# Optimization experiments

Measured on AMD Instinct MI355X. Metric: run time of the kernel, lower is better.

The kernel has to match this reference:

```python
import jax, jax.numpy as jnp
import numpy as np

N = 131072      # total nodes across batched molecular graphs
E = 524288      # directed edges (avg degree ~4)
G = 4096        # number of graphs in the batch
C_IN = 78       # atom feature dim
C_OUT = 128


def _init_linear(key, fan_in, fan_out):
    kw, kb = jax.random.split(key)
    s = 1.0 / np.sqrt(fan_in)
    W = jax.random.uniform(kw, (fan_in, fan_out), jnp.float32, -s, s)
    b = jax.random.uniform(kb, (fan_out,), jnp.float32, -s, s)
    return W, b


def setup_inputs() -> dict:
    key = jax.random.key(0)
    ks = jax.random.split(key, 8)
    x = jax.random.normal(ks[0], (N, C_IN), jnp.float32)
    edge_index = jax.random.randint(ks[1], (2, E), 0, N, dtype=jnp.int32)
    # sorted graph assignment, every graph non-empty (32 nodes per graph)
    batch = ((jnp.arange(N, dtype=jnp.int32) * G) // N).astype(jnp.int32)
    W1, b1 = _init_linear(ks[2], C_IN, C_IN)
    W2, b2 = _init_linear(ks[3], C_IN, 2 * C_IN)
    W3, b3 = _init_linear(ks[4], 2 * C_IN, 4 * C_IN)
    fcW, fcb = _init_linear(ks[5], 4 * C_IN, C_OUT)
    return {"x": x, "edge_index": edge_index, "batch": batch,
            "W1": W1, "b1": b1, "W2": W2, "b2": b2,
            "W3": W3, "b3": b3, "fcW": fcW, "fcb": fcb}


def _gcn_norm(edge_index, n):
    # PyG gcn_norm: add self-loops (weight 1), symmetric D^-1/2 A D^-1/2
    loop = jnp.arange(n, dtype=edge_index.dtype)
    src = jnp.concatenate([edge_index[0], loop])
    dst = jnp.concatenate([edge_index[1], loop])
    deg = jax.ops.segment_sum(jnp.ones_like(dst, jnp.float32), dst, num_segments=n)
    dis = jnp.where(deg > 0, jax.lax.rsqrt(jnp.maximum(deg, 1.0)), 0.0)
    norm = dis[src] * dis[dst]  # [E + N]
    return src, dst, norm


def _gcn_conv(h, W, b, src, dst, norm, n):
    h = h @ W                       # linear transform first (PyG order)
    msg = h[src] * norm[:, None]    # gather + edge-normalize
    agg = jax.ops.segment_sum(msg, dst, num_segments=n)  # scatter-add
    return agg + b


def reference(x, edge_index, batch, W1, b1, W2, b2, W3, b3, fcW, fcb):
    n = x.shape[0]
    src, dst, norm = _gcn_norm(edge_index, n)
    h = jax.nn.relu(_gcn_conv(x, W1, b1, src, dst, norm, n))
    h = jax.nn.relu(_gcn_conv(h, W2, b2, src, dst, norm, n))
    h = jax.nn.relu(_gcn_conv(h, W3, b3, src, dst, norm, n))
    pooled = jax.ops.segment_max(h, batch, num_segments=G)  # global max pool
    out = pooled @ fcW + fcb
    # dropout is identity in eval mode
    return out
```

## Files before the change

### kernel.cpp

```cpp
#include <hip/hip_runtime.h>

#define NN 131072
#define NE 524288
#define NG 4096

typedef __attribute__((ext_vector_type(8))) short bfx8;
typedef __attribute__((ext_vector_type(4))) float f32x4;

static __device__ __forceinline__ ushort f2bf(float f) {
    union { float f; unsigned u; } v; v.f = f;
    unsigned r = (v.u + 0x7fff + ((v.u >> 16) & 1)) >> 16;
    return (ushort)r;
}
static __device__ __forceinline__ float bf2f(short s) {
    union { unsigned u; float f; } v;
    v.u = ((unsigned)(ushort)s) << 16;
    return v.f;
}


__global__ void k_count(const int* __restrict__ dst, int* __restrict__ counts) {
    int e = blockIdx.x * blockDim.x + threadIdx.x;
    if (e < NE) atomicAdd(&counts[dst[e]], 1);
}

__global__ void k_dis(const int* __restrict__ counts, float* __restrict__ dis) {
    int i = blockIdx.x * blockDim.x + threadIdx.x;
    if (i < NN) dis[i] = rsqrtf((float)(counts[i] + 1));
}

__global__ void k_scanA(const int* __restrict__ in, int* __restrict__ out, int* __restrict__ bsum) {
    __shared__ int s[256];
    int t = threadIdx.x;
    int i = blockIdx.x * 256 + t;
    int v = in[i];
    s[t] = v;
    __syncthreads();
    for (int off = 1; off < 256; off <<= 1) {
        int x = (t >= off) ? s[t - off] : 0;
        __syncthreads();
        s[t] += x;
        __syncthreads();
    }
    out[i] = s[t] - v;
    if (t == 255) bsum[blockIdx.x] = s[t];
}

__global__ void k_scanB(int* __restrict__ bsum) {
    __shared__ int s[512];
    int t = threadIdx.x;
    int v = bsum[t];
    s[t] = v;
    __syncthreads();
    for (int off = 1; off < 512; off <<= 1) {
        int x = (t >= off) ? s[t - off] : 0;
        __syncthreads();
        s[t] += x;
        __syncthreads();
    }
    bsum[t] = s[t] - v;
}

__global__ void k_scanC(int* __restrict__ rowstart, const int* __restrict__ bsum) {
    int t = threadIdx.x;
    int i = blockIdx.x * 256 + t;
    rowstart[i] += bsum[blockIdx.x];
    if (i == 0) rowstart[NN] = NE;
}

__global__ void k_fill(const int* __restrict__ src, const int* __restrict__ dst,
                       const int* __restrict__ rowstart, int* __restrict__ cursor,
                       const float* __restrict__ dis,
                       int* __restrict__ col, float* __restrict__ wgt) {
    int e = blockIdx.x * blockDim.x + threadIdx.x;
    if (e >= NE) return;
    int s = src[e], d = dst[e];
    int pos = rowstart[d] + atomicAdd(&cursor[d], 1);
    col[pos] = s;
    wgt[pos] = dis[s] * dis[d];
}

template<int CI, int CO, int KP>
__global__ void k_prepW(const float* __restrict__ W, ushort* __restrict__ WT) {
    int idx = blockIdx.x * 256 + threadIdx.x;
    if (idx >= CO * KP) return;
    int n = idx / KP, k = idx - n * KP;
    float v = (k < CI) ? W[k * CO + n] : 0.0f;
    WT[idx] = f2bf(v);
}

__global__ void k_prepX(const float* __restrict__ x, ushort* __restrict__ xb) {
    int idx = blockIdx.x * 256 + threadIdx.x;
    int i = idx / 96, c = idx - i * 96;
    xb[idx] = (c < 78) ? f2bf(x[i * 78 + c]) : (ushort)0;
}


template<int CP>
__global__ __launch_bounds__(256)
void k_agg8(const ushort* __restrict__ hin, const int* __restrict__ rowstart,
            const int* __restrict__ col, const float* __restrict__ wgt,
            const float* __restrict__ dis, ushort* __restrict__ out) {
    constexpr int CH = CP / 8;
    int idx = blockIdx.x * 256 + threadIdx.x;
    int i = idx / CH;
    int ch = (idx - i * CH) * 8;
    const ushort* base = hin + ch;

    float d = dis[i];
    bfx8 self = *(const bfx8*)(hin + (size_t)i * CP + ch);
    float acc[8];
    #pragma unroll
    for (int k = 0; k < 8; ++k) acc[k] = d * d * bf2f(self[k]);

    int j = rowstart[i], j1 = rowstart[i + 1];
    for (; j + 4 <= j1; j += 4) {
        int c0 = col[j], c1 = col[j + 1], c2 = col[j + 2], c3 = col[j + 3];
        float w0 = wgt[j], w1 = wgt[j + 1], w2 = wgt[j + 2], w3 = wgt[j + 3];
        bfx8 g0 = *(const bfx8*)(base + (size_t)c0 * CP);
        bfx8 g1 = *(const bfx8*)(base + (size_t)c1 * CP);
        bfx8 g2 = *(const bfx8*)(base + (size_t)c2 * CP);
        bfx8 g3 = *(const bfx8*)(base + (size_t)c3 * CP);
        #pragma unroll
        for (int k = 0; k < 8; ++k) {
            acc[k] = fmaf(w0, bf2f(g0[k]), acc[k]);
            acc[k] = fmaf(w1, bf2f(g1[k]), acc[k]);
            acc[k] = fmaf(w2, bf2f(g2[k]), acc[k]);
            acc[k] = fmaf(w3, bf2f(g3[k]), acc[k]);
        }
    }
    for (; j < j1; ++j) {
        int c = col[j];
        float w = wgt[j];
        bfx8 g = *(const bfx8*)(base + (size_t)c * CP);
        #pragma unroll
        for (int k = 0; k < 8; ++k) acc[k] = fmaf(w, bf2f(g[k]), acc[k]);
    }

    bfx8 ov;
    #pragma unroll
    for (int k = 0; k < 8; ++k) ov[k] = (short)f2bf(acc[k]);
    *(bfx8*)(out + (size_t)i * CP + ch) = ov;
}


template<int KP, int LCH, int CO, int CPO, bool POOL>
__global__ __launch_bounds__(256)
void k_mfma(const ushort* __restrict__ A, const ushort* __restrict__ BT,
            const float* __restrict__ bias, const int* __restrict__ batch,
            ushort* __restrict__ hout, float* __restrict__ pooled) {
    constexpr int NCH = KP / 8;
    constexpr int LP  = LCH * 8;
    constexpr int NP  = (CO + 63) / 64;
    __shared__ ushort sA[64 * LP];

    const int tid  = threadIdx.x;
    const int row0 = blockIdx.x * 64;

    for (int id = tid; id < 64 * NCH; id += 256) {
        int r = id / NCH, kc = id - r * NCH;
        int swz = (kc & ~7) | ((kc & 7) ^ (r & 7));
        ((int4*)(sA + r * LP))[swz] = ((const int4*)(A + (size_t)(row0 + r) * KP))[kc];
    }
    __syncthreads();

    const int lane = tid & 63;
    const int wave = tid >> 6;
    const int wr = wave >> 1, wc = wave & 1;
    const int l15 = lane & 15, l4 = lane >> 4;
    const int r7 = l15 & 7;
    const int rowA0 = wr * 32 + l15;
    const int gbase = row0 + wr * 32;
    const int koff = l4 * 8;

    #pragma unroll
    for (int p = 0; p < NP; ++p) {
        const int bc0 = p * 64 + wc * 32 + l15;
        f32x4 acc[2][2] = {};
        #pragma unroll
        for (int ks = 0; ks < KP / 32; ++ks) {
            int chunk = l4 + ks * 4;
            int swz = (chunk & ~7) | ((chunk & 7) ^ r7);
            int off = swz * 8;
            bfx8 a0 = *(const bfx8*)(sA + rowA0 * LP + off);
            bfx8 a1 = *(const bfx8*)(sA + (rowA0 + 16) * LP + off);
            bfx8 b0 = {0,0,0,0,0,0,0,0}, b1 = {0,0,0,0,0,0,0,0};
            if (bc0 < CO)      b0 = *(const bfx8*)(BT + (size_t)bc0 * KP + koff + ks * 32);
            if (bc0 + 16 < CO) b1 = *(const bfx8*)(BT + (size_t)(bc0 + 16) * KP + koff + ks * 32);
            acc[0][0] = __builtin_amdgcn_mfma_f32_16x16x32_bf16(a0, b0, acc[0][0], 0, 0, 0);
            acc[0][1] = __builtin_amdgcn_mfma_f32_16x16x32_bf16(a0, b1, acc[0][1], 0, 0, 0);
            acc[1][0] = __builtin_amdgcn_mfma_f32_16x16x32_bf16(a1, b0, acc[1][0], 0, 0, 0);
            acc[1][1] = __builtin_amdgcn_mfma_f32_16x16x32_bf16(a1, b1, acc[1][1], 0, 0, 0);
        }

        if constexpr (POOL) {
            const bool uni = (batch[gbase] == batch[gbase + 31]);
            #pragma unroll
            for (int fn = 0; fn < 2; ++fn) {
                int cg = p * 64 + wc * 32 + fn * 16 + l15;
                bool cok = cg < CO;
                float bs = cok ? bias[cg] : 0.0f;
                if (uni) {
                    float m = -1e30f;
                    #pragma unroll
                    for (int fm = 0; fm < 2; ++fm)
                        #pragma unroll
                        for (int j = 0; j < 4; ++j)
                            m = fmaxf(m, acc[fm][fn][j]);
                    m = fmaxf(m, __shfl_xor(m, 16));
                    m = fmaxf(m, __shfl_xor(m, 32));
                    if (l4 == 0 && cok) {
                        int g = batch[gbase];
                        float v = fmaxf(m + bs, 0.0f);
                        atomicMax((int*)&pooled[g * CO + cg], __float_as_int(v));
                    }
                } else {
                    #pragma unroll
                    for (int fm = 0; fm < 2; ++fm)
                        #pragma unroll
                        for (int j = 0; j < 4; ++j) {
                            if (cok) {
                                int rg = gbase + fm * 16 + l4 * 4 + j;
                                int g = batch[rg];
                                float v = fmaxf(acc[fm][fn][j] + bs, 0.0f);
                                atomicMax((int*)&pooled[g * CO + cg], __float_as_int(v));
                            }
                        }
                }
            }
        } else {
            #pragma unroll
            for (int fn = 0; fn < 2; ++fn) {
                int cg = p * 64 + wc * 32 + fn * 16 + l15;
                if (cg >= CPO) continue;
                float bs = (cg < CO) ? bias[cg] : 0.0f;
                #pragma unroll
                for (int fm = 0; fm < 2; ++fm)
                    #pragma unroll
                    for (int j = 0; j < 4; ++j) {
                        int row = gbase + fm * 16 + l4 * 4 + j;
                        float v = (cg < CO) ? fmaxf(acc[fm][fn][j] + bs, 0.0f) : 0.0f;
                        hout[(size_t)row * CPO + cg] = f2bf(v);
                    }
            }
        }
    }
}


__global__ __launch_bounds__(256)
void k_fc(const float* __restrict__ pooled, const float* __restrict__ fcW,
          const float* __restrict__ fcb, float* __restrict__ out) {
    __shared__ float sp[8][312];
    const int tid = threadIdx.x;
    const int g0 = blockIdx.x * 8;

    for (int k = tid; k < 8 * 312; k += 256)
        ((float*)sp)[k] = pooled[(size_t)g0 * 312 + k];
    __syncthreads();

    const int half = tid >> 7;
    const int c = tid & 127;
    float b = fcb[c];
    float acc0 = b, acc1 = b, acc2 = b, acc3 = b;
    const float* wp = fcW + c;
    const float* p0 = sp[half * 4 + 0];
    const float* p1 = sp[half * 4 + 1];
    const float* p2 = sp[half * 4 + 2];
    const float* p3 = sp[half * 4 + 3];
    #pragma unroll 4
    for (int k = 0; k < 312; ++k) {
        float w = wp[(size_t)k * 128];
        acc0 = fmaf(p0[k], w, acc0);
        acc1 = fmaf(p1[k], w, acc1);
        acc2 = fmaf(p2[k], w, acc2);
        acc3 = fmaf(p3[k], w, acc3);
    }
    float* o = out + (size_t)(g0 + half * 4) * 128 + c;
    o[0] = acc0; o[128] = acc1; o[256] = acc2; o[384] = acc3;
}


extern "C" void kernel_launch(void* const* d_in, const int* in_sizes, int n_in,
                              void* d_out, int out_size, void* d_ws, size_t ws_size,
                              hipStream_t stream) {
    const float* x    = (const float*)d_in[0];
    const int*   ei   = (const int*)d_in[1];
    const int*   srcv = ei;
    const int*   dstv = ei + NE;
    const int*   batch = (const int*)d_in[2];
    const float* W1 = (const float*)d_in[3];
    const float* b1 = (const float*)d_in[4];
    const float* W2 = (const float*)d_in[5];
    const float* b2 = (const float*)d_in[6];
    const float* W3 = (const float*)d_in[7];
    const float* b3 = (const float*)d_in[8];
    const float* fcW = (const float*)d_in[9];
    const float* fcb = (const float*)d_in[10];
    float* out = (float*)d_out;

    char* ws = (char*)d_ws;
    size_t off = 0;
    auto take = [&](size_t bytes) -> void* {
        void* p = ws + off;
        off += (bytes + 255) & ~(size_t)255;
        return p;
    };
    int*    counts   = (int*)take((size_t)NN * 4);
    int*    rowstart = (int*)take((size_t)(NN + 1) * 4);
    int*    cursor   = (int*)take((size_t)NN * 4);
    float*  dis      = (float*)take((size_t)NN * 4);
    int*    bsum     = (int*)take(512 * 4);
    int*    col      = (int*)take((size_t)NE * 4);
    float*  wgt      = (float*)take((size_t)NE * 4);
    ushort* R1       = (ushort*)take((size_t)NN * 160 * 2);
    ushort* R2       = (ushort*)take((size_t)NN * 160 * 2);
    ushort* R3       = (ushort*)take((size_t)NN * 96 * 2);
    float*  pooled   = (float*)take((size_t)NG * 312 * 4);
    ushort* W1T      = (ushort*)take((size_t)78 * 96 * 2);
    ushort* W2T      = (ushort*)take((size_t)156 * 96 * 2);
    ushort* W3T      = (ushort*)take((size_t)312 * 160 * 2);

    ushort* xb = R1;
    ushort* A1 = R2;
    ushort* h1 = R3;
    ushort* A2 = R1;
    ushort* h2 = R2;
    ushort* A3 = R1;

    hipMemsetAsync(counts, 0, (size_t)NN * 4, stream);
    hipMemsetAsync(cursor, 0, (size_t)NN * 4, stream);
    hipMemsetAsync(pooled, 0, (size_t)NG * 312 * 4, stream);

    k_count<<<NE / 256, 256, 0, stream>>>(dstv, counts);
    k_dis<<<NN / 256, 256, 0, stream>>>(counts, dis);
    k_scanA<<<NN / 256, 256, 0, stream>>>(counts, rowstart, bsum);
    k_scanB<<<1, 512, 0, stream>>>(bsum);
    k_scanC<<<NN / 256, 256, 0, stream>>>(rowstart, bsum);
    k_fill<<<NE / 256, 256, 0, stream>>>(srcv, dstv, rowstart, cursor, dis, col, wgt);

    k_prepW<78, 78, 96><<<(78 * 96 + 255) / 256, 256, 0, stream>>>(W1, W1T);
    k_prepW<78, 156, 96><<<(156 * 96 + 255) / 256, 256, 0, stream>>>(W2, W2T);
    k_prepW<156, 312, 160><<<(312 * 160 + 255) / 256, 256, 0, stream>>>(W3, W3T);
    k_prepX<<<NN * 96 / 256, 256, 0, stream>>>(x, xb);

    k_agg8<96><<<NN * 12 / 256, 256, 0, stream>>>(xb, rowstart, col, wgt, dis, A1);
    k_mfma<96, 16, 78, 96, false><<<NN / 64, 256, 0, stream>>>(A1, W1T, b1, nullptr, h1, nullptr);
    k_agg8<96><<<NN * 12 / 256, 256, 0, stream>>>(h1, rowstart, col, wgt, dis, A2);
    k_mfma<96, 16, 156, 160, false><<<NN / 64, 256, 0, stream>>>(A2, W2T, b2, nullptr, h2, nullptr);
    k_agg8<160><<<NN * 20 / 256, 256, 0, stream>>>(h2, rowstart, col, wgt, dis, A3);
    k_mfma<160, 24, 312, 312, true><<<NN / 64, 256, 0, stream>>>(A3, W3T, b3, batch, nullptr, pooled);
    k_fc<<<NG / 8, 256, 0, stream>>>(pooled, fcW, fcb, out);
}
```

Baseline: 381.0 us.

## Fuse neighbor aggregation into MFMA GEMM kernel via shared-memory staging

The sparse aggregation step is now computed directly inside each GEMM block. Each thread gathers neighbor rows, accumulates them, and writes the aggregated bf16 tile into the swizzled shared-memory A tile, with no separate aggregate buffer in global memory. This removes one kernel launch per layer and a full write and re-read of the aggregated activations. In exchange, the gather phase now runs with the GEMM block's occupancy and thread mapping (64 rows per block), which may give less latency hiding for the irregular gathers.

```diff
diff --git a/kernel.cpp b/kernel.cpp
--- a/kernel.cpp
+++ b/kernel.cpp
@@ -96,59 +96,14 @@
 }
 
 
-template<int CP>
-__global__ __launch_bounds__(256)
-void k_agg8(const ushort* __restrict__ hin, const int* __restrict__ rowstart,
-            const int* __restrict__ col, const float* __restrict__ wgt,
-            const float* __restrict__ dis, ushort* __restrict__ out) {
-    constexpr int CH = CP / 8;
-    int idx = blockIdx.x * 256 + threadIdx.x;
-    int i = idx / CH;
-    int ch = (idx - i * CH) * 8;
-    const ushort* base = hin + ch;
-
-    float d = dis[i];
-    bfx8 self = *(const bfx8*)(hin + (size_t)i * CP + ch);
-    float acc[8];
-    #pragma unroll
-    for (int k = 0; k < 8; ++k) acc[k] = d * d * bf2f(self[k]);
-
-    int j = rowstart[i], j1 = rowstart[i + 1];
-    for (; j + 4 <= j1; j += 4) {
-        int c0 = col[j], c1 = col[j + 1], c2 = col[j + 2], c3 = col[j + 3];
-        float w0 = wgt[j], w1 = wgt[j + 1], w2 = wgt[j + 2], w3 = wgt[j + 3];
-        bfx8 g0 = *(const bfx8*)(base + (size_t)c0 * CP);
-        bfx8 g1 = *(const bfx8*)(base + (size_t)c1 * CP);
-        bfx8 g2 = *(const bfx8*)(base + (size_t)c2 * CP);
-        bfx8 g3 = *(const bfx8*)(base + (size_t)c3 * CP);
-        #pragma unroll
-        for (int k = 0; k < 8; ++k) {
-            acc[k] = fmaf(w0, bf2f(g0[k]), acc[k]);
-            acc[k] = fmaf(w1, bf2f(g1[k]), acc[k]);
-            acc[k] = fmaf(w2, bf2f(g2[k]), acc[k]);
-            acc[k] = fmaf(w3, bf2f(g3[k]), acc[k]);
-        }
-    }
-    for (; j < j1; ++j) {
-        int c = col[j];
-        float w = wgt[j];
-        bfx8 g = *(const bfx8*)(base + (size_t)c * CP);
-        #pragma unroll
-        for (int k = 0; k < 8; ++k) acc[k] = fmaf(w, bf2f(g[k]), acc[k]);
-    }
-
-    bfx8 ov;
-    #pragma unroll
-    for (int k = 0; k < 8; ++k) ov[k] = (short)f2bf(acc[k]);
-    *(bfx8*)(out + (size_t)i * CP + ch) = ov;
-}
-
-
 template<int KP, int LCH, int CO, int CPO, bool POOL>
 __global__ __launch_bounds__(256)
-void k_mfma(const ushort* __restrict__ A, const ushort* __restrict__ BT,
-            const float* __restrict__ bias, const int* __restrict__ batch,
-            ushort* __restrict__ hout, float* __restrict__ pooled) {
+void k_fused(const ushort* __restrict__ hin, const int* __restrict__ rowstart,
+             const int* __restrict__ col, const float* __restrict__ wgt,
+             const float* __restrict__ dis,
+             const ushort* __restrict__ BT, const float* __restrict__ bias,
+             const int* __restrict__ batch,
+             ushort* __restrict__ hout, float* __restrict__ pooled) {
     constexpr int NCH = KP / 8;
     constexpr int LP  = LCH * 8;
     constexpr int NP  = (CO + 63) / 64;
@@ -158,9 +113,46 @@
     const int row0 = blockIdx.x * 64;
 
     for (int id = tid; id < 64 * NCH; id += 256) {
-        int r = id / NCH, kc = id - r * NCH;
+        int r  = id / NCH, kc = id - r * NCH;
+        int i  = row0 + r;
+        int ch = kc * 8;
+        const ushort* gb = hin + ch;
+
+        float d = dis[i];
+        bfx8 self = *(const bfx8*)(hin + (size_t)i * KP + ch);
+        float acc[8];
+        #pragma unroll
+        for (int k = 0; k < 8; ++k) acc[k] = d * d * bf2f(self[k]);
+
+        int j = rowstart[i], j1 = rowstart[i + 1];
+        for (; j + 4 <= j1; j += 4) {
+            int c0 = col[j], c1 = col[j + 1], c2 = col[j + 2], c3 = col[j + 3];
+            float w0 = wgt[j], w1 = wgt[j + 1], w2 = wgt[j + 2], w3 = wgt[j + 3];
+            bfx8 g0 = *(const bfx8*)(gb + (size_t)c0 * KP);
+            bfx8 g1 = *(const bfx8*)(gb + (size_t)c1 * KP);
+            bfx8 g2 = *(const bfx8*)(gb + (size_t)c2 * KP);
+            bfx8 g3 = *(const bfx8*)(gb + (size_t)c3 * KP);
+            #pragma unroll
+            for (int k = 0; k < 8; ++k) {
+                acc[k] = fmaf(w0, bf2f(g0[k]), acc[k]);
+                acc[k] = fmaf(w1, bf2f(g1[k]), acc[k]);
+                acc[k] = fmaf(w2, bf2f(g2[k]), acc[k]);
+                acc[k] = fmaf(w3, bf2f(g3[k]), acc[k]);
+            }
+        }
+        for (; j < j1; ++j) {
+            int c = col[j];
+            float w = wgt[j];
+            bfx8 g = *(const bfx8*)(gb + (size_t)c * KP);
+            #pragma unroll
+            for (int k = 0; k < 8; ++k) acc[k] = fmaf(w, bf2f(g[k]), acc[k]);
+        }
+
+        bfx8 ov;
+        #pragma unroll
+        for (int k = 0; k < 8; ++k) ov[k] = (short)f2bf(acc[k]);
         int swz = (kc & ~7) | ((kc & 7) ^ (r & 7));
-        ((int4*)(sA + r * LP))[swz] = ((const int4*)(A + (size_t)(row0 + r) * KP))[kc];
+        *(bfx8*)(sA + r * LP + swz * 8) = ov;
     }
     __syncthreads();
 
@@ -313,20 +305,13 @@
     int*    bsum     = (int*)take(512 * 4);
     int*    col      = (int*)take((size_t)NE * 4);
     float*  wgt      = (float*)take((size_t)NE * 4);
-    ushort* R1       = (ushort*)take((size_t)NN * 160 * 2);
-    ushort* R2       = (ushort*)take((size_t)NN * 160 * 2);
-    ushort* R3       = (ushort*)take((size_t)NN * 96 * 2);
+    ushort* xb       = (ushort*)take((size_t)NN * 96 * 2);
+    ushort* h1       = (ushort*)take((size_t)NN * 96 * 2);
+    ushort* h2       = (ushort*)take((size_t)NN * 160 * 2);
     float*  pooled   = (float*)take((size_t)NG * 312 * 4);
     ushort* W1T      = (ushort*)take((size_t)78 * 96 * 2);
     ushort* W2T      = (ushort*)take((size_t)156 * 96 * 2);
     ushort* W3T      = (ushort*)take((size_t)312 * 160 * 2);
-
-    ushort* xb = R1;
-    ushort* A1 = R2;
-    ushort* h1 = R3;
-    ushort* A2 = R1;
-    ushort* h2 = R2;
-    ushort* A3 = R1;
 
     hipMemsetAsync(counts, 0, (size_t)NN * 4, stream);
     hipMemsetAsync(cursor, 0, (size_t)NN * 4, stream);
@@ -344,11 +329,12 @@
     k_prepW<156, 312, 160><<<(312 * 160 + 255) / 256, 256, 0, stream>>>(W3, W3T);
     k_prepX<<<NN * 96 / 256, 256, 0, stream>>>(x, xb);
 
-    k_agg8<96><<<NN * 12 / 256, 256, 0, stream>>>(xb, rowstart, col, wgt, dis, A1);
-    k_mfma<96, 16, 78, 96, false><<<NN / 64, 256, 0, stream>>>(A1, W1T, b1, nullptr, h1, nullptr);
-    k_agg8<96><<<NN * 12 / 256, 256, 0, stream>>>(h1, rowstart, col, wgt, dis, A2);
-    k_mfma<96, 16, 156, 160, false><<<NN / 64, 256, 0, stream>>>(A2, W2T, b2, nullptr, h2, nullptr);
-    k_agg8<160><<<NN * 20 / 256, 256, 0, stream>>>(h2, rowstart, col, wgt, dis, A3);
-    k_mfma<160, 24, 312, 312, true><<<NN / 64, 256, 0, stream>>>(A3, W3T, b3, batch, nullptr, pooled);
+    k_fused<96, 16, 78, 96, false><<<NN / 64, 256, 0, stream>>>(
+        xb, rowstart, col, wgt, dis, W1T, b1, nullptr, h1, nullptr);
+    k_fused<96, 16, 156, 160, false><<<NN / 64, 256, 0, stream>>>(
+        h1, rowstart, col, wgt, dis, W2T, b2, nullptr, h2, nullptr);
+    k_fused<160, 24, 312, 312, true><<<NN / 64, 256, 0, stream>>>(
+        h2, rowstart, col, wgt, dis, W3T, b3, batch, nullptr, pooled);
+
     k_fc<<<NG / 8, 256, 0, stream>>>(pooled, fcW, fcb, out);
 }
```

After: 356.9 us. 6.3% less time.
